# Performance work log

Measured on AMD Instinct MI355X. Metric: run time of the kernel, lower is better.

The kernel has to match this reference:

```python
import jax, jax.numpy as jnp
import numpy as np

B, N, D = 8, 2048, 1024
DQ, DV = 1024, 1024


def setup_inputs() -> dict:
    key = jax.random.key(0)
    ks = jax.random.split(key, 7)
    s = 1.0 / np.sqrt(D)
    return {
        "x": jax.random.normal(ks[0], (B, N, D), dtype=jnp.float32),
        "Wq": jax.random.uniform(ks[1], (D, DQ), jnp.float32, -s, s),
        "bq": jax.random.uniform(ks[2], (DQ,), jnp.float32, -s, s),
        "Wk": jax.random.uniform(ks[3], (D, DQ), jnp.float32, -s, s),
        "bk": jax.random.uniform(ks[4], (DQ,), jnp.float32, -s, s),
        "Wv": jax.random.uniform(ks[5], (D, DV), jnp.float32, -s, s),
        "bv": jax.random.uniform(ks[6], (DV,), jnp.float32, -s, s),
    }


def reference(x, Wq, bq, Wk, bk, Wv, bv):
    # Linear projections (nn.Linear: x @ W + b)
    Q = jnp.einsum("bnd,dq->bnq", x, Wq) + bq  # [B,N,DQ]
    K = jnp.einsum("bnd,dq->bnq", x, Wk) + bk  # [B,N,DQ]
    V = jnp.einsum("bnd,dv->bnv", x, Wv) + bv  # [B,N,DV]
    # NOTE: original forward does NOT apply the 1/sqrt(dk) scaling.
    scores = jnp.einsum("bnq,bmq->bnm", Q, K)  # [B,N,N]
    attn = jax.nn.softmax(scores, axis=-1)
    out = jnp.einsum("bnm,bmv->bnv", attn, V)  # [B,N,DV]
    return out
```

## Files before the change

kernel.cpp:

```cpp
#include <hip/hip_runtime.h>
#include <hip/hip_bf16.h>
#include <stdint.h>


typedef _Float16 f16;
typedef _Float16 f16x8 __attribute__((ext_vector_type(8)));
typedef _Float16 f16x4 __attribute__((ext_vector_type(4)));
typedef float f32x4 __attribute__((ext_vector_type(4)));

typedef __attribute__((address_space(3))) void lds_void;
typedef const __attribute__((address_space(1))) void gbl_void;

__device__ __forceinline__ void async16(void* l, const void* g) {
    __builtin_amdgcn_global_load_lds(
        reinterpret_cast<gbl_void*>(reinterpret_cast<uintptr_t>(g)),
        reinterpret_cast<lds_void*>(reinterpret_cast<uintptr_t>(l)),
        16, 0, 0);
}

__global__ __launch_bounds__(256) void cast_f32_f16(const float* __restrict__ x,
                                                    f16* __restrict__ y) {
    long i = (long)blockIdx.x * 256 + threadIdx.x;
    float4 v = reinterpret_cast<const float4*>(x)[i];
    f16x4 o = {(f16)v.x, (f16)v.y, (f16)v.z, (f16)v.w};
    reinterpret_cast<f16x4*>(y)[i] = o;
}

__global__ __launch_bounds__(256) void transpose_cast3(const float* __restrict__ W0,
                                                       const float* __restrict__ W1,
                                                       const float* __restrict__ W2,
                                                       f16* __restrict__ wt) {
    const float* W = blockIdx.z == 0 ? W0 : blockIdx.z == 1 ? W1 : W2;
    f16* o = wt + (long)blockIdx.z * 1024 * 1024;
    __shared__ float tile[32][33];
    int c0 = blockIdx.x * 32, r0 = blockIdx.y * 32;
    int tx = threadIdx.x, ty = threadIdx.y;
#pragma unroll
    for (int i = ty; i < 32; i += 8) tile[i][tx] = W[(long)(r0 + i) * 1024 + c0 + tx];
    __syncthreads();
#pragma unroll
    for (int i = ty; i < 32; i += 8) o[(long)(c0 + i) * 1024 + r0 + tx] = (f16)tile[tx][i];
}

template <int MODE>
__global__ __launch_bounds__(512, 2) void gemm256(
    const f16* __restrict__ A, const f16* __restrict__ Bm,
    f16* __restrict__ o16, float* __restrict__ o32,
    const float* __restrict__ bq, const float* __restrict__ bk,
    const float* __restrict__ bv,
    f16* __restrict__ Qo, f16* __restrict__ Ko, f16* __restrict__ Vto) {
    constexpr int LDA = MODE == 2 ? 2048 : 1024;
    constexpr int LDB = MODE == 2 ? 2048 : 1024;
    constexpr int NT = (MODE == 2 ? 2048 : 1024) / 64;

    __shared__ f16 sm[65536];
    char* smb = (char*)sm;

    const int tid = threadIdx.x;
    const int lane = tid & 63;
    const int wv = tid >> 6;
    const int wmi = wv >> 2;
    const int wni = wv & 3;

    const int L = blockIdx.x;
    long mBase, nBase, oOff = 0;
    int nx = 0;
    if (MODE == 0) {
        const int xcd = L & 7, j = L >> 3;
        nx = j >> 3;
        mBase = (long)(xcd * 8 + (j & 7)) * 256;
        nBase = (long)nx * 256;
    } else if (MODE == 1) {
        const int b = L & 7, j = L >> 3;
        mBase = (long)(j & 7) * 256;
        nBase = (long)(j >> 3) * 256;
        A += (long)b * 2048 * 1024;
        Bm += (long)b * 2048 * 1024;
        oOff = (long)b * 2048 * 2048;
    } else {
        const int b = L & 7, j = L >> 3;
        mBase = (long)(j & 7) * 256;
        nBase = (long)(j >> 3) * 256;
        A += (long)b * 2048 * 2048;
        Bm += (long)b * 1024 * 2048;
        oOff = (long)b * 2048 * 1024;
    }

    const int sru = tid >> 3;
    const int sck = (tid & 7) ^ (sru & 7);
    const f16* pA = A + (mBase + sru) * LDA + sck * 8;
    const f16* pB = Bm + (nBase + sru) * LDB + sck * 8;

    auto stA = [&](int bufB, int half, int t) {
        const f16* s = pA + half * 128 * LDA + t * 64;
        char* d = smb + bufB + half * 16384 + tid * 16;
        async16(d, s);
        async16(d + 8192, s + 64 * LDA);
    };
    auto stB = [&](int bufB, int half, int t) {
        const f16* s = pB + half * 128 * LDB + t * 64;
        char* d = smb + bufB + 32768 + half * 16384 + tid * 16;
        async16(d, s);
        async16(d + 8192, s + 64 * LDB);
    };

    const int pc0 = (lane >> 4) ^ (lane & 7);
    const int aBase = (wmi * 128 + (lane & 15)) * 64 + pc0 * 8;
    const int bBase = 16384 + (wni * 64 + (lane & 15)) * 64 + pc0 * 8;

    f32x4 acc[8][4] = {};
    f16x8 aX[4], bX[4], aY[4], bY[4];

    auto rdA = [&](f16x8* dst, int cE, int mh, int ksx) {
#pragma unroll
        for (int i = 0; i < 4; ++i)
            dst[i] = *reinterpret_cast<const f16x8*>(
                &sm[cE + ((aBase + (mh * 4 + i) * 1024) ^ ksx)]);
    };
    auto rdB = [&](f16x8* dst, int cE, int ksx) {
#pragma unroll
        for (int q = 0; q < 4; ++q)
            dst[q] = *reinterpret_cast<const f16x8*>(
                &sm[cE + ((bBase + q * 1024) ^ ksx)]);
    };
    auto mm = [&](int mh, const f16x8* a, const f16x8* b) {
        __builtin_amdgcn_s_setprio(1);
#pragma unroll
        for (int i = 0; i < 4; ++i)
#pragma unroll
            for (int nf = 0; nf < 4; ++nf)
                acc[mh * 4 + i][nf] = __builtin_amdgcn_mfma_f32_16x16x32_f16(
                    a[i], b[nf], acc[mh * 4 + i][nf], 0, 0, 0);
        __builtin_amdgcn_s_setprio(0);
    };

    stA(0, 0, 0); stA(0, 1, 0); stB(0, 0, 0); stB(0, 1, 0);
    stA(65536, 0, 1); stA(65536, 1, 1); stB(65536, 0, 1);
    asm volatile("s_waitcnt vmcnt(6)" ::: "memory");
    __builtin_amdgcn_s_barrier();
    rdA(aX, 0, 0, 0); rdB(bX, 0, 0);

    for (int t = 0; t < NT; ++t) {
        const int cE = (t & 1) << 15;
        const int cB = (t & 1) << 16;
        const int nB = cB ^ 65536;
        rdA(aY, cE, 1, 0); rdB(bY, cE, 0);
        if (t + 1 < NT) stB(nB, 1, t + 1);
        mm(0, aX, bX);
        __builtin_amdgcn_s_barrier();
        rdA(aX, cE, 0, 32); rdB(bX, cE, 32);
        mm(1, aY, bY);
        __builtin_amdgcn_s_barrier();
        rdA(aY, cE, 1, 32); rdB(bY, cE, 32);
        mm(0, aX, bX);
        __builtin_amdgcn_s_barrier();
        asm volatile("s_waitcnt vmcnt(0)" ::: "memory");
        if (t + 1 < NT) {
            rdA(aX, cE ^ 32768, 0, 0); rdB(bX, cE ^ 32768, 0);
            asm volatile("s_waitcnt lgkmcnt(8)" ::: "memory");
        } else {
            asm volatile("s_waitcnt lgkmcnt(0)" ::: "memory");
        }
        if (t + 2 < NT) { stA(cB, 0, t + 2); stA(cB, 1, t + 2); stB(cB, 0, t + 2); }
        mm(1, aY, bY);
        __builtin_amdgcn_s_barrier();
    }

    const int rq = (lane >> 4) * 4;
    const int cl = lane & 15;
    if (MODE == 0) {
        const int seg = nx >> 2;
        const float* bias = seg == 0 ? bq : seg == 1 ? bk : bv;
        f16* outQK = seg == 0 ? Qo : Ko;
#pragma unroll
        for (int mf = 0; mf < 8; ++mf)
#pragma unroll
            for (int nf = 0; nf < 4; ++nf) {
                const long c = (nBase & 1023) + wni * 64 + nf * 16 + cl;
                const float bb = bias[c];
#pragma unroll
                for (int r = 0; r < 4; ++r) {
                    const long row = mBase + wmi * 128 + mf * 16 + rq + r;
                    const float v = acc[mf][nf][r] + bb;
                    if (seg < 2) {
                        outQK[row * 1024 + c] = (f16)v;
                    } else {
                        Vto[((row >> 11) * 1024 + c) * 2048 + (row & 2047)] = (f16)v;
                    }
                }
            }
    } else if (MODE == 1) {
        f16* o = o16 + oOff;
#pragma unroll
        for (int mf = 0; mf < 8; ++mf)
#pragma unroll
            for (int nf = 0; nf < 4; ++nf) {
                const long col = nBase + wni * 64 + nf * 16 + cl;
#pragma unroll
                for (int r = 0; r < 4; ++r) {
                    const long row = mBase + wmi * 128 + mf * 16 + rq + r;
                    o[row * 2048 + col] = (f16)acc[mf][nf][r];
                }
            }
    } else {
        float* o = o32 + oOff;
#pragma unroll
        for (int mf = 0; mf < 8; ++mf)
#pragma unroll
            for (int nf = 0; nf < 4; ++nf) {
                const long col = nBase + wni * 64 + nf * 16 + cl;
#pragma unroll
                for (int r = 0; r < 4; ++r) {
                    const long row = mBase + wmi * 128 + mf * 16 + rq + r;
                    o[row * 1024 + col] = acc[mf][nf][r];
                }
            }
    }
}

__global__ __launch_bounds__(256) void softmax_rows(const f16* __restrict__ S,
                                                    f16* __restrict__ P) {
    const long row = blockIdx.x;
    const int t = threadIdx.x;
    f16x8 a = reinterpret_cast<const f16x8*>(S + row * 2048)[t];
    float e[8];
    float m = -1e30f;
#pragma unroll
    for (int j = 0; j < 8; ++j) { e[j] = (float)a[j]; m = fmaxf(m, e[j]); }
#pragma unroll
    for (int o = 32; o > 0; o >>= 1) m = fmaxf(m, __shfl_down(m, o, 64));
    __shared__ float red[8];
    if ((t & 63) == 0) red[t >> 6] = m;
    __syncthreads();
    m = fmaxf(fmaxf(red[0], red[1]), fmaxf(red[2], red[3]));
    float s = 0.0f;
#pragma unroll
    for (int j = 0; j < 8; ++j) { e[j] = __expf(e[j] - m); s += e[j]; }
#pragma unroll
    for (int o = 32; o > 0; o >>= 1) s += __shfl_down(s, o, 64);
    if ((t & 63) == 0) red[4 + (t >> 6)] = s;
    __syncthreads();
    s = red[4] + red[5] + red[6] + red[7];
    float inv = 1.0f / s;
    f16x8 o;
#pragma unroll
    for (int j = 0; j < 8; ++j) o[j] = (f16)(e[j] * inv);
    reinterpret_cast<f16x8*>(P + row * 2048)[t] = o;
}

extern "C" void kernel_launch(void* const* d_in, const int* in_sizes, int n_in,
                              void* d_out, int out_size, void* d_ws, size_t ws_size,
                              hipStream_t stream) {
    const float* x  = (const float*)d_in[0];
    const float* Wq = (const float*)d_in[1];
    const float* bq = (const float*)d_in[2];
    const float* Wk = (const float*)d_in[3];
    const float* bk = (const float*)d_in[4];
    const float* Wv = (const float*)d_in[5];
    const float* bv = (const float*)d_in[6];
    float* out = (float*)d_out;
    char* ws = (char*)d_ws;

    f16* Q   = (f16*)(ws + 0);
    f16* Kb  = (f16*)(ws + 33554432);
    f16* Vt  = (f16*)(ws + 67108864);
    f16* S16 = (f16*)(ws + 100663296);
    f16* P   = (f16*)(ws + 167772160);
    f16* xh  = (f16*)(ws + 100663296);
    f16* wt  = (f16*)(ws + 134217728);

    cast_f32_f16<<<16384, 256, 0, stream>>>(x, xh);
    transpose_cast3<<<dim3(32, 32, 3), dim3(32, 8), 0, stream>>>(Wq, Wk, Wv, wt);

    gemm256<0><<<768, 512, 0, stream>>>(xh, wt, nullptr, nullptr,
                                        bq, bk, bv, Q, Kb, Vt);

    gemm256<1><<<512, 512, 0, stream>>>(Q, Kb, S16, nullptr,
                                        nullptr, nullptr, nullptr,
                                        nullptr, nullptr, nullptr);

    softmax_rows<<<16384, 256, 0, stream>>>(S16, P);

    gemm256<2><<<256, 512, 0, stream>>>(P, Vt, nullptr, out,
                                        nullptr, nullptr, nullptr,
                                        nullptr, nullptr, nullptr);
}
```

Baseline: 417.1 us.

## Restructure GEMM main loop into four-phase schedule with larger A fragment reuse

Replaces the ping-pong register schedule (4 A and 4 B fragments split into halves) with a per-tile macro that loads all 8 A fragments per k-half and streams B fragments in pairs. Global-to-LDS async stores are interleaved across four MFMA phases, separated by barriers and explicit lgkmcnt/vmcnt waits. The loop is unrolled by two so the buffer offsets are compile-time constants. The aim is better overlap of LDS reads, global prefetch and MFMA. The cost is more barriers and higher register pressure from holding 16 A fragments, and the loop assumes an even NT.

```diff
diff --git a/kernel.cpp b/kernel.cpp
--- a/kernel.cpp
+++ b/kernel.cpp
@@ -108,63 +108,74 @@
     const int aBase = (wmi * 128 + (lane & 15)) * 64 + pc0 * 8;
     const int bBase = 16384 + (wni * 64 + (lane & 15)) * 64 + pc0 * 8;
 
-    f32x4 acc[8][4] = {};
-    f16x8 aX[4], bX[4], aY[4], bY[4];
-
-    auto rdA = [&](f16x8* dst, int cE, int mh, int ksx) {
-#pragma unroll
-        for (int i = 0; i < 4; ++i)
-            dst[i] = *reinterpret_cast<const f16x8*>(
-                &sm[cE + ((aBase + (mh * 4 + i) * 1024) ^ ksx)]);
-    };
-    auto rdB = [&](f16x8* dst, int cE, int ksx) {
-#pragma unroll
-        for (int q = 0; q < 4; ++q)
-            dst[q] = *reinterpret_cast<const f16x8*>(
-                &sm[cE + ((bBase + q * 1024) ^ ksx)]);
-    };
-    auto mm = [&](int mh, const f16x8* a, const f16x8* b) {
-        __builtin_amdgcn_s_setprio(1);
-#pragma unroll
-        for (int i = 0; i < 4; ++i)
-#pragma unroll
-            for (int nf = 0; nf < 4; ++nf)
-                acc[mh * 4 + i][nf] = __builtin_amdgcn_mfma_f32_16x16x32_f16(
-                    a[i], b[nf], acc[mh * 4 + i][nf], 0, 0, 0);
-        __builtin_amdgcn_s_setprio(0);
-    };
-
     stA(0, 0, 0); stA(0, 1, 0); stB(0, 0, 0); stB(0, 1, 0);
     stA(65536, 0, 1); stA(65536, 1, 1); stB(65536, 0, 1);
     asm volatile("s_waitcnt vmcnt(6)" ::: "memory");
     __builtin_amdgcn_s_barrier();
-    rdA(aX, 0, 0, 0); rdB(bX, 0, 0);
-
-    for (int t = 0; t < NT; ++t) {
-        const int cE = (t & 1) << 15;
-        const int cB = (t & 1) << 16;
-        const int nB = cB ^ 65536;
-        rdA(aY, cE, 1, 0); rdB(bY, cE, 0);
-        if (t + 1 < NT) stB(nB, 1, t + 1);
-        mm(0, aX, bX);
-        __builtin_amdgcn_s_barrier();
-        rdA(aX, cE, 0, 32); rdB(bX, cE, 32);
-        mm(1, aY, bY);
-        __builtin_amdgcn_s_barrier();
-        rdA(aY, cE, 1, 32); rdB(bY, cE, 32);
-        mm(0, aX, bX);
-        __builtin_amdgcn_s_barrier();
-        asm volatile("s_waitcnt vmcnt(0)" ::: "memory");
-        if (t + 1 < NT) {
-            rdA(aX, cE ^ 32768, 0, 0); rdB(bX, cE ^ 32768, 0);
-            asm volatile("s_waitcnt lgkmcnt(8)" ::: "memory");
-        } else {
-            asm volatile("s_waitcnt lgkmcnt(0)" ::: "memory");
-        }
-        if (t + 2 < NT) { stA(cB, 0, t + 2); stA(cB, 1, t + 2); stB(cB, 0, t + 2); }
-        mm(1, aY, bY);
-        __builtin_amdgcn_s_barrier();
-    }
+
+    f32x4 acc[8][4] = {};
+
+#define GTILE(T, CE, CB, NB)                                                      \
+    {                                                                             \
+        const int t_ = (T);                                                       \
+        f16x8 a0[8], a1[8], bA[2], bB[2], bC[2], bD[2];                           \
+        _Pragma("unroll") for (int mf = 0; mf < 8; ++mf)                          \
+            a0[mf] = *reinterpret_cast<const f16x8*>(&sm[(CE) + aBase + mf * 1024]); \
+        _Pragma("unroll") for (int q = 0; q < 2; ++q)                             \
+            bA[q] = *reinterpret_cast<const f16x8*>(&sm[(CE) + bBase + q * 1024]); \
+        _Pragma("unroll") for (int mf = 0; mf < 8; ++mf)                          \
+            a1[mf] = *reinterpret_cast<const f16x8*>(&sm[(CE) + ((aBase + mf * 1024) ^ 32)]); \
+        if (t_ + 1 < NT) stB((NB), 1, t_ + 1);                                    \
+        __builtin_amdgcn_s_barrier();                                             \
+        asm volatile("s_waitcnt lgkmcnt(8)" ::: "memory");                        \
+        _Pragma("unroll") for (int mf = 0; mf < 8; ++mf) {                        \
+            acc[mf][0] = __builtin_amdgcn_mfma_f32_16x16x32_f16(a0[mf], bA[0], acc[mf][0], 0, 0, 0); \
+            acc[mf][1] = __builtin_amdgcn_mfma_f32_16x16x32_f16(a0[mf], bA[1], acc[mf][1], 0, 0, 0); \
+        }                                                                         \
+        asm volatile("s_waitcnt lgkmcnt(0)" ::: "memory");                        \
+        __builtin_amdgcn_s_barrier();                                             \
+        _Pragma("unroll") for (int q = 0; q < 2; ++q)                             \
+            bB[q] = *reinterpret_cast<const f16x8*>(&sm[(CE) + bBase + (2 + q) * 1024]); \
+        if (t_ + 2 < NT) stA((CB), 0, t_ + 2);                                    \
+        __builtin_amdgcn_s_barrier();                                             \
+        asm volatile("s_waitcnt lgkmcnt(0)" ::: "memory");                        \
+        _Pragma("unroll") for (int mf = 0; mf < 8; ++mf) {                        \
+            acc[mf][2] = __builtin_amdgcn_mfma_f32_16x16x32_f16(a0[mf], bB[0], acc[mf][2], 0, 0, 0); \
+            acc[mf][3] = __builtin_amdgcn_mfma_f32_16x16x32_f16(a0[mf], bB[1], acc[mf][3], 0, 0, 0); \
+        }                                                                         \
+        __builtin_amdgcn_s_barrier();                                             \
+        _Pragma("unroll") for (int q = 0; q < 2; ++q)                             \
+            bC[q] = *reinterpret_cast<const f16x8*>(&sm[(CE) + ((bBase + q * 1024) ^ 32)]); \
+        _Pragma("unroll") for (int q = 0; q < 2; ++q)                             \
+            bD[q] = *reinterpret_cast<const f16x8*>(&sm[(CE) + ((bBase + (2 + q) * 1024) ^ 32)]); \
+        if (t_ + 2 < NT) stA((CB), 1, t_ + 2);                                    \
+        __builtin_amdgcn_s_barrier();                                             \
+        asm volatile("s_waitcnt lgkmcnt(2)" ::: "memory");                        \
+        _Pragma("unroll") for (int mf = 0; mf < 8; ++mf) {                        \
+            acc[mf][0] = __builtin_amdgcn_mfma_f32_16x16x32_f16(a1[mf], bC[0], acc[mf][0], 0, 0, 0); \
+            acc[mf][1] = __builtin_amdgcn_mfma_f32_16x16x32_f16(a1[mf], bC[1], acc[mf][1], 0, 0, 0); \
+        }                                                                         \
+        asm volatile("s_waitcnt lgkmcnt(0)" ::: "memory");                        \
+        __builtin_amdgcn_s_barrier();                                             \
+        if (t_ + 2 < NT) stB((CB), 0, t_ + 2);                                    \
+        __builtin_amdgcn_s_barrier();                                             \
+        _Pragma("unroll") for (int mf = 0; mf < 8; ++mf) {                        \
+            acc[mf][2] = __builtin_amdgcn_mfma_f32_16x16x32_f16(a1[mf], bD[0], acc[mf][2], 0, 0, 0); \
+            acc[mf][3] = __builtin_amdgcn_mfma_f32_16x16x32_f16(a1[mf], bD[1], acc[mf][3], 0, 0, 0); \
+        }                                                                         \
+        if (t_ < NT - 2) {                                                        \
+            asm volatile("s_waitcnt vmcnt(6)" ::: "memory");                      \
+        } else {                                                                  \
+            asm volatile("s_waitcnt vmcnt(0)" ::: "memory");                      \
+        }                                                                         \
+        __builtin_amdgcn_s_barrier();                                             \
+    }
+
+    for (int tt = 0; tt < NT; tt += 2) {
+        GTILE(tt, 0, 0, 65536)
+        GTILE(tt + 1, 32768, 65536, 0)
+    }
+#undef GTILE
 
     const int rq = (lane >> 4) * 4;
     const int cl = lane & 15;
```

Result: slower. 444.7 us (+6.6%).
